# Optimization experiments

Hardware: AMD Instinct MI355X
Metric: run time of the kernel (lower is better)

## Reference

```python
import jax, jax.numpy as jnp
import numpy as np

EPS = 1e-8
LRELU_SLOPE = 0.2


def leaky_relu(x, p=LRELU_SLOPE):
    return jnp.where(x >= 0, x, p * x)


def conv2dmod(x, weight, style):
    """StyleGAN2 weight-demodulated conv.
    x: [B,C_in,H,W], weight: [C_out,C_in,k,k], style: [B,C_in]."""
    # per-sample modulation: scale input channels by (style + 1)
    w = weight[None] * (style[:, None, :, None, None] + 1.0)  # [B,O,I,k,k]
    # demodulation: rescale each output filter to unit norm
    d = jax.lax.rsqrt(jnp.sum(w * w, axis=(2, 3, 4), keepdims=True) + EPS)
    w = w * d

    def conv_one(xi, wi):
        # xi: [C_in,H,W], wi: [O,I,k,k] -> [O,H,W]
        return jax.lax.conv_general_dilated(
            xi[None], wi, window_strides=(1, 1), padding='SAME',
            dimension_numbers=('NCHW', 'OIHW', 'NCHW'))[0]

    return jax.vmap(conv_one)(x, w)  # [B,O,H,W]


def setup_inputs() -> dict:
    key = jax.random.key(0)
    ks = jax.random.split(key, 9)
    B, C_in, C_out, H, W = 16, 128, 256, 128, 128
    return {
        "features": jax.random.normal(ks[0], (B, C_in, H, W), jnp.float32),
        "style_mean1": jax.random.normal(ks[1], (B, C_in, 1, 1), jnp.float32),
        "style_std1": jax.random.normal(ks[2], (B, C_in, 1, 1), jnp.float32),
        "style_mean2": jax.random.normal(ks[3], (B, C_in, 1, 1), jnp.float32),
        "style_std2": jax.random.normal(ks[4], (B, C_in, 1, 1), jnp.float32),
        "lastBlockBool": 0,
        "w1": jax.random.normal(ks[5], (C_in, C_in, 3, 3), jnp.float32),
        "w2": jax.random.normal(ks[6], (C_in, C_in, 3, 3), jnp.float32),
        "down_w": jax.random.normal(ks[7], (C_out, C_in, 4, 4), jnp.float32) * 0.05,
        "down_b": jnp.zeros((C_out,), jnp.float32),
    }


def reference(features, style_mean1, style_std1, style_mean2, style_std2,
              lastBlockBool, w1, w2, down_w, down_b):
    # style_mean2/style_std2/lastBlockBool are accepted but unused by the
    # original forward; dropout is identity (eval mode).
    s1 = style_mean1[:, :, 0, 0]  # squeeze(-1).squeeze(-1) -> [B,C_in]
    s2 = style_std1[:, :, 0, 0]
    x = leaky_relu(conv2dmod(features, w1, s1))
    x = leaky_relu(conv2dmod(x, w2, s2) + x)  # residual
    # downsample: 4x4 conv, stride 2, pad 1 -> halves H,W
    y = jax.lax.conv_general_dilated(
        x, down_w, window_strides=(2, 2), padding=((1, 1), (1, 1)),
        dimension_numbers=('NCHW', 'OIHW', 'NCHW'))
    return y + down_b[None, :, None, None]
```

## Files before the change

### kernel.cpp

```cpp
#include <hip/hip_runtime.h>
#include <hip/hip_bf16.h>

constexpr int B  = 16;
constexpr int C  = 128;
constexpr int H  = 128;
constexpr int W  = 128;
constexpr int CO = 256;
constexpr int HO = 64;
constexpr int WO = 64;

#define EPSV   1e-8f
#define SLOPE  0.2f

typedef short bf16x8 __attribute__((ext_vector_type(8)));
typedef float f32x4  __attribute__((ext_vector_type(4)));

typedef const __attribute__((address_space(1))) unsigned int  gbl_u32;
typedef __attribute__((address_space(3))) unsigned int        lds_u32;

__device__ __forceinline__ short f2bs(float v) {
    __hip_bfloat16 h = __float2bfloat16(v);
    return *(short*)&h;
}
__device__ __forceinline__ float bs2f(short s) {
    __hip_bfloat16 h = *(__hip_bfloat16*)&s;
    return __bfloat162float(h);
}

__global__ __launch_bounds__(128) void demod_kernel(
    const float* __restrict__ w1, const float* __restrict__ w2,
    const float* __restrict__ s1, const float* __restrict__ s2,
    float* __restrict__ d)
{
    int bid  = blockIdx.x;
    int conv = bid >> 11;
    int b    = (bid >> 7) & 15;
    int o    = bid & 127;
    const float* w = conv ? w2 : w1;
    const float* s = conv ? s2 : s1;
    int i = threadIdx.x;
    float sv = s[b * C + i] + 1.0f;
    const float* wp = w + (o * C + i) * 9;
    float sum = 0.f;
    #pragma unroll
    for (int k = 0; k < 9; ++k) { float t = wp[k] * sv; sum += t * t; }
    #pragma unroll
    for (int off = 32; off; off >>= 1) sum += __shfl_down(sum, off);
    __shared__ float red[2];
    if ((threadIdx.x & 63) == 0) red[threadIdx.x >> 6] = sum;
    __syncthreads();
    if (threadIdx.x == 0) d[bid] = rsqrtf(red[0] + red[1] + EPSV);
}

__global__ __launch_bounds__(256) void expand_kernel(
    const float* __restrict__ w1, const float* __restrict__ w2,
    const float* __restrict__ s1, const float* __restrict__ s2,
    const float* __restrict__ d, short* __restrict__ wm)
{
    int idx = blockIdx.x * 256 + threadIdx.x;
    int ic  = idx & 127;
    int oc  = (idx >> 7) & 127;
    int t   = idx >> 14;
    int tap = t % 9;
    int cb  = t / 9;
    int b   = cb & 15;
    int conv= cb >> 4;
    const float* w = conv ? w2 : w1;
    const float* s = conv ? s2 : s1;
    float v = w[(oc * C + ic) * 9 + tap] * (s[b * C + ic] + 1.0f)
            * d[(conv * B + b) * C + oc];
    int icH = ic >> 6, icL = (ic >> 5) & 1;
    int dst = cb * 147456
            + ((icH * 18 + tap * 2 + icL) * 8 + (oc >> 4)) * 512
            + ((ic >> 3) & 3) * 128 + (oc & 15) * 8 + (ic & 7);
    wm[dst] = f2bs(v);
}

__global__ __launch_bounds__(256) void dwexpand_kernel(
    const float* __restrict__ dw, short* __restrict__ dwm)
{
    int idx = blockIdx.x * 256 + threadIdx.x;
    int ic  = idx & 127;
    int oc  = (idx >> 7) & 255;
    int tap = idx >> 15;
    int dst = ((ic >> 5) * 16 + tap) * 8192 + (oc >> 4) * 512
            + ((ic >> 3) & 3) * 128 + (oc & 15) * 8 + (ic & 7);
    dwm[dst] = f2bs(dw[(oc * C + ic) * 16 + tap]);
}

__global__ __launch_bounds__(256) void nchw2nhwc_kernel(
    const float* __restrict__ in, short* __restrict__ out)
{
    __shared__ short s[128 * 136];
    int bid = blockIdx.x;
    int h = bid & 127, b = bid >> 7;
    int tid = threadIdx.x;
    for (int i = tid; i < 128 * 32; i += 256) {
        int w4 = i & 31, ic = i >> 5;
        float4 v = *(const float4*)&in[((b * C + ic) * H + h) * W + w4 * 4];
        s[(w4 * 4 + 0) * 136 + ic] = f2bs(v.x);
        s[(w4 * 4 + 1) * 136 + ic] = f2bs(v.y);
        s[(w4 * 4 + 2) * 136 + ic] = f2bs(v.z);
        s[(w4 * 4 + 3) * 136 + ic] = f2bs(v.w);
    }
    __syncthreads();
    for (int i = tid; i < 128 * 16; i += 256) {
        int icg = i & 15, w = i >> 4;
        *(uint4*)&out[((b * H + h) * W + w) * C + icg * 8] =
            *(uint4*)&s[w * 136 + icg * 8];
    }
}

__global__ __launch_bounds__(256, 4) void conv3x3_mfma(
    const short* __restrict__ in, const short* __restrict__ wmc,
    const short* __restrict__ res, short* __restrict__ out)
{
    __shared__ short sIn[180 * 64];
    __shared__ short sW[2][4096];

    int bid = blockIdx.x;
    int wt = bid & 7, ht = (bid >> 3) & 15, b = bid >> 7;
    int w0 = wt * 16, h0 = ht * 8;
    int tid  = threadIdx.x;
    int lane = tid & 63, wv = tid >> 6;
    int q = lane >> 4, l15 = lane & 15;
    int wr = wv & 1;
    int wc = wv >> 1;

    const short* wb = wmc + b * 147456;

    auto stageIn = [&](int st) {
        for (int i = tid; i < 180 * 8; i += 256) {
            int slot = i & 7, pix = i >> 3;
            int hl = pix / 18, wl = pix - hl * 18;
            int gh = h0 - 1 + hl, gw = w0 - 1 + wl;
            uint4 v = make_uint4(0u, 0u, 0u, 0u);
            if ((unsigned)gh < (unsigned)H && (unsigned)gw < (unsigned)W)
                v = *(const uint4*)&in[((b * H + gh) * W + gw) * C + st * 64 + slot * 8];
            *(uint4*)&sIn[pix * 64 + ((slot ^ (pix & 7)) << 3)] = v;
        }
    };
    auto stageW = [&](int st, int s, int buf) {
        #pragma unroll
        for (int i = 0; i < 2; ++i) {
            const short* g = wb + st * 73728 + s * 4096
                           + (wv * 2 + i) * 512 + lane * 8;
            __builtin_amdgcn_global_load_lds(
                (gbl_u32*)g, (lds_u32*)&sW[buf][(wv * 2 + i) * 512], 16, 0, 0);
        }
    };

    f32x4 acc[4][4];
    #pragma unroll
    for (int mt = 0; mt < 4; ++mt)
        #pragma unroll
        for (int nt = 0; nt < 4; ++nt)
            acc[mt][nt] = (f32x4){0.f, 0.f, 0.f, 0.f};

    stageW(0, 0, 0);
    stageIn(0);
    __syncthreads();

    int bfbase = q * 128 + l15 * 8;

    #pragma unroll 1
    for (int st = 0; st < 2; ++st) {
        #pragma unroll 2
        for (int s = 0; s < 18; ++s) {
            int tap = s >> 1, icL = s & 1;
            int dh = tap / 3, dwd = tap - dh * 3;
            if (s < 17)        stageW(st, s + 1, (s + 1) & 1);
            else if (st == 0)  stageW(1, 0, 0);
            bf16x8 af[4], bf[4];
            #pragma unroll
            for (int mt = 0; mt < 4; ++mt) {
                int pix  = (wr * 4 + mt + dh) * 18 + l15 + dwd;
                int slot = (icL * 4 + q) ^ (pix & 7);
                af[mt] = *(const bf16x8*)&sIn[pix * 64 + slot * 8];
            }
            #pragma unroll
            for (int nt = 0; nt < 4; ++nt)
                bf[nt] = *(const bf16x8*)&sW[s & 1][(wc * 4 + nt) * 512 + bfbase];
            #pragma unroll
            for (int mt = 0; mt < 4; ++mt)
                #pragma unroll
                for (int nt = 0; nt < 4; ++nt)
                    acc[mt][nt] = __builtin_amdgcn_mfma_f32_16x16x32_bf16(
                        af[mt], bf[nt], acc[mt][nt], 0, 0, 0);
            __syncthreads();
        }
        if (st == 0) { stageIn(1); __syncthreads(); }
    }

    bool has_res = (res != nullptr);
    #pragma unroll
    for (int mt = 0; mt < 4; ++mt) {
        int h = h0 + wr * 4 + mt;
        #pragma unroll
        for (int nt = 0; nt < 4; ++nt) {
            int oc = wc * 64 + nt * 16 + l15;
            #pragma unroll
            for (int reg = 0; reg < 4; ++reg) {
                int w = w0 + q * 4 + reg;
                int idx = ((b * H + h) * W + w) * C + oc;
                float v = acc[mt][nt][reg];
                if (has_res) v += bs2f(res[idx]);
                v = v >= 0.f ? v : SLOPE * v;
                out[idx] = f2bs(v);
            }
        }
    }
}

__global__ __launch_bounds__(256, 3) void downconv_mfma(
    const short* __restrict__ in, const short* __restrict__ dwm,
    const float* __restrict__ db, float* __restrict__ out)
{
    __shared__ short sIn[340 * 32];
    __shared__ short sW[2][8192];

    int bid = blockIdx.x;
    int wt = bid & 3;  bid >>= 2;
    int ht = bid & 15; bid >>= 4;
    int b  = bid;
    int ow0 = wt * 16, oh0 = ht * 4;
    int ih0 = 2 * oh0 - 1, iw0 = 2 * ow0 - 1;

    int tid  = threadIdx.x;
    int lane = tid & 63, wv = tid >> 6;
    int q = lane >> 4, l15 = lane & 15;

    auto stageIn = [&](int icC) {
        for (int i = tid; i < 340 * 4; i += 256) {
            int slot = i & 3, pix = i >> 2;
            int ihl = pix / 34, iwl = pix - ihl * 34;
            int gh = ih0 + ihl, gw = iw0 + iwl;
            uint4 v = make_uint4(0u, 0u, 0u, 0u);
            if ((unsigned)gh < (unsigned)H && (unsigned)gw < (unsigned)W)
                v = *(const uint4*)&in[((b * H + gh) * W + gw) * C + icC * 32 + slot * 8];
            int par = iwl & 1, col = iwl >> 1;
            int pl  = ihl * 17 + col;
            *(uint4*)&sIn[(par * 170 + pl) * 32 + ((slot ^ ((pl >> 1) & 3)) << 3)] = v;
        }
    };
    auto stageW = [&](int step, int buf) {
        #pragma unroll
        for (int j = 0; j < 4; ++j) {
            int base = (j * 4 + wv) * 512;
            const short* g = dwm + step * 8192 + base + lane * 8;
            __builtin_amdgcn_global_load_lds(
                (gbl_u32*)g, (lds_u32*)&sW[buf][base], 16, 0, 0);
        }
    };

    f32x4 acc[4][4];
    #pragma unroll
    for (int mt = 0; mt < 4; ++mt)
        #pragma unroll
        for (int nt = 0; nt < 4; ++nt)
            acc[mt][nt] = (f32x4){0.f, 0.f, 0.f, 0.f};

    stageW(0, 0);
    stageIn(0);
    __syncthreads();

    int afbase = q * 128 + l15 * 8;

    #pragma unroll 1
    for (int icC = 0; icC < 4; ++icC) {
        #pragma unroll 2
        for (int tap = 0; tap < 16; ++tap) {
            int step = icC * 16 + tap;
            int buf  = tap & 1;
            if (step < 63) stageW(step + 1, buf ^ 1);
            int dh = tap >> 2, dwn = tap & 3;
            int par = dwn & 1, cb0 = dwn >> 1;
            bf16x8 af[4], bf[4];
            #pragma unroll
            for (int mt = 0; mt < 4; ++mt)
                af[mt] = *(const bf16x8*)&sW[buf][(wv * 4 + mt) * 512 + afbase];
            #pragma unroll
            for (int nt = 0; nt < 4; ++nt) {
                int pl = (2 * nt + dh) * 17 + cb0 + l15;
                bf[nt] = *(const bf16x8*)&sIn[(par * 170 + pl) * 32
                                              + ((q ^ ((pl >> 1) & 3)) << 3)];
            }
            #pragma unroll
            for (int mt = 0; mt < 4; ++mt)
                #pragma unroll
                for (int nt = 0; nt < 4; ++nt)
                    acc[mt][nt] = __builtin_amdgcn_mfma_f32_16x16x32_bf16(
                        af[mt], bf[nt], acc[mt][nt], 0, 0, 0);
            __syncthreads();
        }
        if (icC < 3) { stageIn(icC + 1); __syncthreads(); }
    }

    #pragma unroll
    for (int mt = 0; mt < 4; ++mt) {
        f32x4 bi = *(const f32x4*)&db[wv * 64 + mt * 16 + q * 4];
        #pragma unroll
        for (int nt = 0; nt < 4; ++nt) {
            int oh = oh0 + nt;
            #pragma unroll
            for (int reg = 0; reg < 4; ++reg) {
                int oc = wv * 64 + mt * 16 + q * 4 + reg;
                out[((b * CO + oc) * HO + oh) * WO + ow0 + l15] =
                    acc[mt][nt][reg] + bi[reg];
            }
        }
    }
}

extern "C" void kernel_launch(void* const* d_in, const int* in_sizes, int n_in,
                              void* d_out, int out_size, void* d_ws, size_t ws_size,
                              hipStream_t stream) {
    const float* features = (const float*)d_in[0];
    const float* sm1      = (const float*)d_in[1];
    const float* ss1      = (const float*)d_in[2];
    const float* w1       = (const float*)d_in[6];
    const float* w2       = (const float*)d_in[7];
    const float* dw       = (const float*)d_in[8];
    const float* db       = (const float*)d_in[9];
    float* out = (float*)d_out;

    char* ws = (char*)d_ws;
    short* x1  = (short*)ws;
    short* x2  = (short*)(ws + 67108864);
    short* wm  = (short*)(ws + 134217728);
    short* dwm = (short*)(ws + 143654912);
    float* dv  = (float*)(ws + 144703488);

    demod_kernel    <<<4096, 128, 0, stream>>>(w1, w2, sm1, ss1, dv);
    expand_kernel   <<<18432, 256, 0, stream>>>(w1, w2, sm1, ss1, dv, wm);
    dwexpand_kernel <<<2048, 256, 0, stream>>>(dw, dwm);
    nchw2nhwc_kernel<<<2048, 256, 0, stream>>>(features, x2);
    conv3x3_mfma    <<<2048, 256, 0, stream>>>(x2, wm, nullptr, x1);
    conv3x3_mfma    <<<2048, 256, 0, stream>>>(x1, wm + 16 * 147456, x1, x2);
    downconv_mfma   <<<1024, 256, 0, stream>>>(x2, dwm, db, out);
}
```

Before: 345.4 us.

## Retile downsample conv over output-channel halves and relax barriers with vmcnt waits

```diff
diff --git a/kernel.cpp b/kernel.cpp
--- a/kernel.cpp
+++ b/kernel.cpp
@@ -17,6 +17,13 @@
 
 typedef const __attribute__((address_space(1))) unsigned int  gbl_u32;
 typedef __attribute__((address_space(3))) unsigned int        lds_u32;
+
+__device__ __forceinline__ void bar_raw() {
+    asm volatile("" ::: "memory");
+    __builtin_amdgcn_s_barrier();
+    asm volatile("" ::: "memory");
+}
+#define WAITV(N) asm volatile("s_waitcnt vmcnt(" #N ")" ::: "memory")
 
 __device__ __forceinline__ short f2bs(float v) {
     __hip_bfloat16 h = __float2bfloat16(v);
@@ -83,7 +90,8 @@
     int ic  = idx & 127;
     int oc  = (idx >> 7) & 255;
     int tap = idx >> 15;
-    int dst = ((ic >> 5) * 16 + tap) * 8192 + (oc >> 4) * 512
+    int dst = ((ic >> 5) * 16 + tap) * 8192 + (oc >> 7) * 4096
+            + ((oc >> 4) & 7) * 512
             + ((ic >> 3) & 3) * 128 + (oc & 15) * 8 + (ic & 7);
     dwm[dst] = f2bs(dw[(oc * C + ic) * 16 + tap]);
 }
@@ -171,6 +179,8 @@
             int dh = tap / 3, dwd = tap - dh * 3;
             if (s < 17)        stageW(st, s + 1, (s + 1) & 1);
             else if (st == 0)  stageW(1, 0, 0);
+            if (st == 1 && s == 17) { WAITV(0); } else { WAITV(2); }
+            bar_raw();
             bf16x8 af[4], bf[4];
             #pragma unroll
             for (int mt = 0; mt < 4; ++mt) {
@@ -187,7 +197,7 @@
                 for (int nt = 0; nt < 4; ++nt)
                     acc[mt][nt] = __builtin_amdgcn_mfma_f32_16x16x32_bf16(
                         af[mt], bf[nt], acc[mt][nt], 0, 0, 0);
-            __syncthreads();
+            bar_raw();
         }
         if (st == 0) { stageIn(1); __syncthreads(); }
     }
@@ -212,52 +222,54 @@
     }
 }
 
-__global__ __launch_bounds__(256, 3) void downconv_mfma(
+__global__ __launch_bounds__(256, 2) void downconv_mfma(
     const short* __restrict__ in, const short* __restrict__ dwm,
     const float* __restrict__ db, float* __restrict__ out)
 {
-    __shared__ short sIn[340 * 32];
-    __shared__ short sW[2][8192];
+    __shared__ short sIn[2 * 306 * 32];
+    __shared__ short sW[2][4096];
 
     int bid = blockIdx.x;
-    int wt = bid & 3;  bid >>= 2;
-    int ht = bid & 15; bid >>= 4;
-    int b  = bid;
-    int ow0 = wt * 16, oh0 = ht * 4;
+    int wt = bid & 3;
+    int ht = (bid >> 2) & 7;
+    int ot = (bid >> 5) & 1;
+    int b  = bid >> 6;
+    int ow0 = wt * 16, oh0 = ht * 8, oc0 = ot * 128;
     int ih0 = 2 * oh0 - 1, iw0 = 2 * ow0 - 1;
 
     int tid  = threadIdx.x;
     int lane = tid & 63, wv = tid >> 6;
     int q = lane >> 4, l15 = lane & 15;
 
+    const short* wbase = dwm + ot * 4096;
+
     auto stageIn = [&](int icC) {
-        for (int i = tid; i < 340 * 4; i += 256) {
+        for (int i = tid; i < 612 * 4; i += 256) {
             int slot = i & 3, pix = i >> 2;
             int ihl = pix / 34, iwl = pix - ihl * 34;
             int gh = ih0 + ihl, gw = iw0 + iwl;
             uint4 v = make_uint4(0u, 0u, 0u, 0u);
             if ((unsigned)gh < (unsigned)H && (unsigned)gw < (unsigned)W)
                 v = *(const uint4*)&in[((b * H + gh) * W + gw) * C + icC * 32 + slot * 8];
-            int par = iwl & 1, col = iwl >> 1;
-            int pl  = ihl * 17 + col;
-            *(uint4*)&sIn[(par * 170 + pl) * 32 + ((slot ^ ((pl >> 1) & 3)) << 3)] = v;
+            int par = iwl & 1, pl = ihl * 17 + (iwl >> 1);
+            *(uint4*)&sIn[(par * 306 + pl) * 32 + ((slot ^ ((pl >> 1) & 3)) << 3)] = v;
         }
     };
     auto stageW = [&](int step, int buf) {
         #pragma unroll
-        for (int j = 0; j < 4; ++j) {
-            int base = (j * 4 + wv) * 512;
-            const short* g = dwm + step * 8192 + base + lane * 8;
+        for (int j = 0; j < 2; ++j) {
+            int base = (wv * 2 + j) * 512;
+            const short* g = wbase + step * 8192 + base + lane * 8;
             __builtin_amdgcn_global_load_lds(
                 (gbl_u32*)g, (lds_u32*)&sW[buf][base], 16, 0, 0);
         }
     };
 
-    f32x4 acc[4][4];
-    #pragma unroll
-    for (int mt = 0; mt < 4; ++mt)
-        #pragma unroll
-        for (int nt = 0; nt < 4; ++nt)
+    f32x4 acc[2][8];
+    #pragma unroll
+    for (int mt = 0; mt < 2; ++mt)
+        #pragma unroll
+        for (int nt = 0; nt < 8; ++nt)
             acc[mt][nt] = (f32x4){0.f, 0.f, 0.f, 0.f};
 
     stageW(0, 0);
@@ -271,40 +283,41 @@
         #pragma unroll 2
         for (int tap = 0; tap < 16; ++tap) {
             int step = icC * 16 + tap;
-            int buf  = tap & 1;
-            if (step < 63) stageW(step + 1, buf ^ 1);
+            if (step < 63) stageW(step + 1, (step + 1) & 1);
+            if (step < 63) { WAITV(2); } else { WAITV(0); }
+            bar_raw();
             int dh = tap >> 2, dwn = tap & 3;
             int par = dwn & 1, cb0 = dwn >> 1;
-            bf16x8 af[4], bf[4];
-            #pragma unroll
-            for (int mt = 0; mt < 4; ++mt)
-                af[mt] = *(const bf16x8*)&sW[buf][(wv * 4 + mt) * 512 + afbase];
-            #pragma unroll
-            for (int nt = 0; nt < 4; ++nt) {
+            bf16x8 af[2], bf[8];
+            #pragma unroll
+            for (int mt = 0; mt < 2; ++mt)
+                af[mt] = *(const bf16x8*)&sW[step & 1][(wv * 2 + mt) * 512 + afbase];
+            #pragma unroll
+            for (int nt = 0; nt < 8; ++nt) {
                 int pl = (2 * nt + dh) * 17 + cb0 + l15;
-                bf[nt] = *(const bf16x8*)&sIn[(par * 170 + pl) * 32
+                bf[nt] = *(const bf16x8*)&sIn[(par * 306 + pl) * 32
                                               + ((q ^ ((pl >> 1) & 3)) << 3)];
             }
             #pragma unroll
-            for (int mt = 0; mt < 4; ++mt)
+            for (int mt = 0; mt < 2; ++mt)
                 #pragma unroll
-                for (int nt = 0; nt < 4; ++nt)
+                for (int nt = 0; nt < 8; ++nt)
                     acc[mt][nt] = __builtin_amdgcn_mfma_f32_16x16x32_bf16(
                         af[mt], bf[nt], acc[mt][nt], 0, 0, 0);
-            __syncthreads();
+            bar_raw();
         }
         if (icC < 3) { stageIn(icC + 1); __syncthreads(); }
     }
 
     #pragma unroll
-    for (int mt = 0; mt < 4; ++mt) {
-        f32x4 bi = *(const f32x4*)&db[wv * 64 + mt * 16 + q * 4];
-        #pragma unroll
-        for (int nt = 0; nt < 4; ++nt) {
+    for (int mt = 0; mt < 2; ++mt) {
+        f32x4 bi = *(const f32x4*)&db[oc0 + (wv * 2 + mt) * 16 + q * 4];
+        #pragma unroll
+        for (int nt = 0; nt < 8; ++nt) {
             int oh = oh0 + nt;
             #pragma unroll
             for (int reg = 0; reg < 4; ++reg) {
-                int oc = wv * 64 + mt * 16 + q * 4 + reg;
+                int oc = oc0 + (wv * 2 + mt) * 16 + q * 4 + reg;
                 out[((b * CO + oc) * HO + oh) * WO + ow0 + l15] =
                     acc[mt][nt][reg] + bi[reg];
             }
```

Result: faster. 327.0 us (-5.3%).
